# Kernel optimization log

Hardware: AMD Instinct MI355X
Metric: run time of the kernel (lower is better)

## Reference

```python
import jax, jax.numpy as jnp
import numpy as np

WINDOW = 128
LOOK_BACK = 1
LOOK_FWD = 0   # causal=True -> look_forward defaults to 0
DIM = 64       # rotary dim == head dim


def look_around(x, backward=LOOK_BACK, forward=LOOK_FWD, pad_value=-1):
    # x: [b, windows, window, ...]; pad along windows axis, concat along axis 2
    w = x.shape[1]
    pad = [(0, 0), (backward, forward)] + [(0, 0)] * (x.ndim - 2)
    px = jnp.pad(x, pad, constant_values=pad_value)
    return jnp.concatenate([px[:, i:i + w] for i in range(forward + backward + 1)], axis=2)


def rotate_half(x):
    h = (x.shape[-1] + 1) // 2  # ceil split, matches torch .split([ceil, floor])
    x1, x2 = x[..., :h], x[..., h:]
    return jnp.concatenate([-x2, x1], axis=-1)


def setup_inputs() -> dict:
    key = jax.random.key(0)
    kq, kk, kv = jax.random.split(key, 3)
    shape = (4, 16, 4096, 64)
    return {
        "q": jax.random.normal(kq, shape, dtype=jnp.float32),
        "k": jax.random.normal(kk, shape, dtype=jnp.float32),
        "v": jax.random.normal(kv, shape, dtype=jnp.float32),
    }


def reference(q, k, v):
    B, H, T, e = q.shape
    b = B * H
    q, k, v = (t.reshape(b, T, e) for t in (q, k, v))

    # sinusoidal rotary embeddings (start_pos = 0)
    inv_freq = 1.0 / (10000.0 ** (jnp.arange(0, DIM, 2, dtype=jnp.float32) / DIM))
    t_idx = jnp.arange(T, dtype=jnp.float32)
    freqs = jnp.einsum('i,j->ij', t_idx, inv_freq)          # [T, DIM/2]
    emb = jnp.concatenate([freqs, freqs], axis=-1)[:, :DIM][None]  # [1, T, DIM]
    cos, sin = jnp.cos(emb), jnp.sin(emb)
    q = q * cos + rotate_half(q) * sin
    k = k * cos + rotate_half(k) * sin

    # T is a multiple of WINDOW so autopad is a no-op
    w = T // WINDOW
    bq, bk, bv = (t.reshape(b, w, WINDOW, e) for t in (q, k, v))
    bk = look_around(bk)   # [b, w, (LB+LF+1)*WINDOW, e], padded with -1 (masked below)
    bv = look_around(bv)

    b_t = jnp.arange(T).reshape(1, w, WINDOW)
    bq_t = b_t
    bq_k = look_around(b_t)  # [1, w, (LB+LF+1)*WINDOW]

    dots = (jnp.einsum('bwie,bwje->bwij', bq.astype(jnp.float32), bk.astype(jnp.float32))
            * (e ** -0.5)).astype(q.dtype)
    mask_value = -jnp.finfo(dots.dtype).max

    # causal mask (exact_windowsize=False)
    causal_mask = bq_t[:, :, :, None] < bq_k[:, :, None, :]
    dots = jnp.where(causal_mask, mask_value, dots)
    # look-around padding mask
    dots = jnp.where((bq_k == -1)[:, :, None, :], mask_value, dots)

    attn = jax.nn.softmax(dots, axis=-1)
    out = jnp.einsum('bwij,bwje->bwie', attn, bv)
    return out.reshape(B, H, T, e)
```

## Files before the change

### kernel.cpp

```cpp
#include <hip/hip_runtime.h>

#define T_LEN 4096
#define DHEAD 64
#define WINSZ 128
#define KVLEN 256
#define NWIN 32
#define NBH 64
#define FLTMAX 3.402823466e38f

typedef float f32x4 __attribute__((ext_vector_type(4)));
typedef short s16x8 __attribute__((ext_vector_type(8)));
typedef short s16x4 __attribute__((ext_vector_type(4)));

__device__ __forceinline__ unsigned short f2b(float x) {
  unsigned u = __builtin_bit_cast(unsigned, x);
  u += 0x7fffu + ((u >> 16) & 1u);
  return (unsigned short)(u >> 16);
}

__global__ void rope_tab_kernel(float* __restrict__ tab) {
  const int idx = blockIdx.x * 256 + threadIdx.x;
  if (idx >= T_LEN * 32) return;
  const int t = idx >> 5;
  const int i = idx & 31;
  const float freq = powf(10000.0f, -(float)i / 32.0f);
  float s, c;
  sincosf((float)t * freq, &s, &c);
  tab[idx] = c;
  tab[T_LEN * 32 + idx] = s;
}

__global__ __launch_bounds__(512, 4) void lattn_kernel(
    const float* __restrict__ qg, const float* __restrict__ kg,
    const float* __restrict__ vg, const float* __restrict__ tab,
    float* __restrict__ outg) {
  __shared__ __align__(16) unsigned short Kl[KVLEN * DHEAD];
  __shared__ __align__(16) unsigned short Vt[DHEAD * KVLEN];

  const int bid = blockIdx.x;
  const int win = bid & (NWIN - 1);
  const int bh  = bid >> 5;
  const int tid = threadIdx.x;
  const int lane = tid & 63;
  const int wv = tid >> 6;
  const int l15 = lane & 15;
  const int g = lane >> 4;

  const size_t base = (size_t)bh * T_LEN * DHEAD;
  const int q0 = win * WINSZ;
  const int k0 = q0 - WINSZ;
  const bool use_tab = (tab != nullptr);
  const float* ct = tab;
  const float* st = tab + T_LEN * 32;

  {
    const int c = tid & 7;
    const int rr = tid >> 3;
    float fr[4];
    if (!use_tab) {
      #pragma unroll
      for (int j = 0; j < 4; ++j)
        fr[j] = powf(10000.0f, -(float)(4 * c + j) / 32.0f);
    }
    #pragma unroll
    for (int p = 0; p < 4; ++p) {
      const int kr = p * 64 + rr;
      const int kt = k0 + kr;
      float xa[4] = {0.f,0.f,0.f,0.f}, xb[4] = {0.f,0.f,0.f,0.f};
      float cs[4], sn[4];
      #pragma unroll
      for (int j = 0; j < 4; ++j) { cs[j] = 1.f; sn[j] = 0.f; }
      if (kt >= 0) {
        const float* kp = kg + base + (size_t)kt * DHEAD + 4 * c;
        *(float4*)xa = *(const float4*)kp;
        *(float4*)xb = *(const float4*)(kp + 32);
        if (use_tab) {
          *(float4*)cs = *(const float4*)(ct + kt * 32 + 4 * c);
          *(float4*)sn = *(const float4*)(st + kt * 32 + 4 * c);
        } else {
          #pragma unroll
          for (int j = 0; j < 4; ++j) sincosf((float)kt * fr[j], &sn[j], &cs[j]);
        }
      }
      unsigned wlo[2], whi[2];
      #pragma unroll
      for (int h = 0; h < 2; ++h) {
        const int j0 = 2 * h, j1 = 2 * h + 1;
        wlo[h] = (unsigned)f2b(xa[j0]*cs[j0] - xb[j0]*sn[j0]) |
                 ((unsigned)f2b(xa[j1]*cs[j1] - xb[j1]*sn[j1]) << 16);
        whi[h] = (unsigned)f2b(xb[j0]*cs[j0] + xa[j0]*sn[j0]) |
                 ((unsigned)f2b(xb[j1]*cs[j1] + xa[j1]*sn[j1]) << 16);
      }
      const int su = (kr & 7) << 3;
      uint2 a = {wlo[0], wlo[1]}, b = {whi[0], whi[1]};
      *(uint2*)&Kl[kr * 64 + ((4 * c) ^ su)] = a;
      *(uint2*)&Kl[kr * 64 + ((4 * c + 32) ^ su)] = b;
    }
  }

  {
    const int c = tid & 15;
    const int rp = tid >> 4;
    #pragma unroll
    for (int p = 0; p < 4; ++p) {
      const int kr = (p * 32 + rp) * 2;
      const int kt = k0 + kr;
      float va[4] = {0.f,0.f,0.f,0.f}, vb[4] = {0.f,0.f,0.f,0.f};
      if (kt >= 0)
        *(float4*)va = *(const float4*)(vg + base + (size_t)kt * DHEAD + 4 * c);
      if (kt + 1 >= 0)
        *(float4*)vb = *(const float4*)(vg + base + (size_t)(kt + 1) * DHEAD + 4 * c);
      #pragma unroll
      for (int j = 0; j < 4; ++j) {
        const int d = 4 * c + j;
        const unsigned val = (unsigned)f2b(va[j]) | ((unsigned)f2b(vb[j]) << 16);
        *(unsigned*)&Vt[d * 256 + (kr ^ ((d & 7) << 3))] = val;
      }
    }
  }

  s16x8 qa[2];
  {
    const int qrow = q0 + wv * 16 + l15;
    const float* qp = qg + base + (size_t)qrow * DHEAD + 8 * g;
    float xa[8], xb[8], cs[8], sn[8];
    *(float4*)&xa[0] = *(const float4*)qp;
    *(float4*)&xa[4] = *(const float4*)(qp + 4);
    *(float4*)&xb[0] = *(const float4*)(qp + 32);
    *(float4*)&xb[4] = *(const float4*)(qp + 36);
    if (use_tab) {
      const float* cp = ct + qrow * 32 + 8 * g;
      const float* sp = st + qrow * 32 + 8 * g;
      *(float4*)&cs[0] = *(const float4*)cp;
      *(float4*)&cs[4] = *(const float4*)(cp + 4);
      *(float4*)&sn[0] = *(const float4*)sp;
      *(float4*)&sn[4] = *(const float4*)(sp + 4);
    } else {
      #pragma unroll
      for (int j = 0; j < 8; ++j) {
        const float f = powf(10000.0f, -(float)(8 * g + j) / 32.0f);
        sincosf((float)qrow * f, &sn[j], &cs[j]);
      }
    }
    #pragma unroll
    for (int j = 0; j < 8; ++j) {
      qa[0][j] = (short)f2b(xa[j]*cs[j] - xb[j]*sn[j]);
      qa[1][j] = (short)f2b(xb[j]*cs[j] + xa[j]*sn[j]);
    }
  }

  __syncthreads();

  s16x8 pa[8];
  {
    f32x4 acc[16];
    #pragma unroll
    for (int nt = 0; nt < 16; ++nt) acc[nt] = f32x4{0.f, 0.f, 0.f, 0.f};
    #pragma unroll
    for (int nt = 0; nt < 16; ++nt) {
      const int krow = nt * 16 + l15;
      const int su = (krow & 7) << 3;
      const s16x8 k0f = *(const s16x8*)&Kl[krow * 64 + ((8 * g) ^ su)];
      const s16x8 k1f = *(const s16x8*)&Kl[krow * 64 + ((8 * g + 32) ^ su)];
      acc[nt] = __builtin_amdgcn_mfma_f32_16x16x32_bf16(k0f, qa[0], acc[nt], 0, 0, 0);
      acc[nt] = __builtin_amdgcn_mfma_f32_16x16x32_bf16(k1f, qa[1], acc[nt], 0, 0, 0);
    }
    const int qloc = wv * 16 + l15;
    float mx = -FLTMAX;
    #pragma unroll
    for (int nt = 0; nt < 16; ++nt) {
      const bool pad = (win == 0) && (nt < 8);
      #pragma unroll
      for (int r = 0; r < 4; ++r) {
        const int kloc = nt * 16 + 4 * g + r;
        const bool msk = pad || (kloc > WINSZ + qloc);
        const float s = msk ? -FLTMAX : acc[nt][r];
        acc[nt][r] = s;
        mx = fmaxf(mx, s);
      }
    }
    mx = fmaxf(mx, __shfl_xor(mx, 16));
    mx = fmaxf(mx, __shfl_xor(mx, 32));
    float den = 0.f;
    #pragma unroll
    for (int nt = 0; nt < 16; ++nt) {
      #pragma unroll
      for (int r = 0; r < 4; ++r) {
        const float pv = __expf(0.125f * (acc[nt][r] - mx));
        acc[nt][r] = pv;
        den += pv;
      }
    }
    den += __shfl_xor(den, 16);
    den += __shfl_xor(den, 32);
    const float inv = 1.0f / den;
    #pragma unroll
    for (int ks = 0; ks < 8; ++ks) {
      #pragma unroll
      for (int j = 0; j < 4; ++j) {
        pa[ks][j]     = (short)f2b(acc[2 * ks][j] * inv);
        pa[ks][j + 4] = (short)f2b(acc[2 * ks + 1][j] * inv);
      }
    }
  }

  f32x4 oacc[4];
  #pragma unroll
  for (int nt = 0; nt < 4; ++nt) oacc[nt] = f32x4{0.f, 0.f, 0.f, 0.f};

  #pragma unroll
  for (int ks = 0; ks < 8; ++ks) {
    #pragma unroll
    for (int nt = 0; nt < 4; ++nt) {
      const int d = nt * 16 + l15;
      const int su = (d & 7) << 3;
      const int c1 = ks * 32 + 4 * g;
      const s16x4 v0 = *(const s16x4*)&Vt[d * 256 + (c1 ^ su)];
      const s16x4 v1 = *(const s16x4*)&Vt[d * 256 + ((c1 + 16) ^ su)];
      const s16x8 vb = __builtin_shufflevector(v0, v1, 0, 1, 2, 3, 4, 5, 6, 7);
      oacc[nt] = __builtin_amdgcn_mfma_f32_16x16x32_bf16(pa[ks], vb, oacc[nt], 0, 0, 0);
    }
  }

  float* op = outg + base;
  #pragma unroll
  for (int r = 0; r < 4; ++r) {
    const int qrow = q0 + wv * 16 + 4 * g + r;
    #pragma unroll
    for (int nt = 0; nt < 4; ++nt)
      op[(size_t)qrow * DHEAD + nt * 16 + l15] = oacc[nt][r];
  }
}

extern "C" void kernel_launch(void* const* d_in, const int* in_sizes, int n_in,
                              void* d_out, int out_size, void* d_ws, size_t ws_size,
                              hipStream_t stream) {
  (void)in_sizes; (void)n_in; (void)out_size;
  const float* q = (const float*)d_in[0];
  const float* k = (const float*)d_in[1];
  const float* v = (const float*)d_in[2];
  float* out = (float*)d_out;

  float* tab = nullptr;
  const size_t tab_bytes = (size_t)2 * T_LEN * 32 * sizeof(float);
  if (ws_size >= tab_bytes) {
    tab = (float*)d_ws;
    rope_tab_kernel<<<dim3((T_LEN * 32 + 255) / 256), dim3(256), 0, stream>>>(tab);
  }
  lattn_kernel<<<dim3(NBH * NWIN), dim3(512), 0, stream>>>(q, k, v, tab, out);
}
```

Measured before the change: 227.3 us.

## Process four consecutive windows per block, reusing staged K/V halves in a ring

Each block now handles four consecutive windows of one head. It keeps the K/V tiles in two 128-row halves, so only one new half is loaded and converted per window instead of the full 256-row look-around. This removes the duplicate global reads and RoPE/bf16 conversion of the shared previous window. Softmax normalisation is also deferred: the output is scaled at store time instead of scaling the probabilities, the bf16 conversion now uses the library intrinsic, and the V swizzle changed. In exchange the grid has four times fewer blocks, and each window iteration serialises on an extra barrier before reloading.

```diff
diff --git a/kernel.cpp b/kernel.cpp
--- a/kernel.cpp
+++ b/kernel.cpp
@@ -1,11 +1,13 @@
 #include <hip/hip_runtime.h>
+#include <hip/hip_bf16.h>
 
 #define T_LEN 4096
 #define DHEAD 64
 #define WINSZ 128
-#define KVLEN 256
 #define NWIN 32
 #define NBH 64
+#define NWPB 4
+#define NGRP (NWIN / NWPB)
 #define FLTMAX 3.402823466e38f
 
 typedef float f32x4 __attribute__((ext_vector_type(4)));
@@ -13,9 +15,7 @@
 typedef short s16x4 __attribute__((ext_vector_type(4)));
 
 __device__ __forceinline__ unsigned short f2b(float x) {
-  unsigned u = __builtin_bit_cast(unsigned, x);
-  u += 0x7fffu + ((u >> 16) & 1u);
-  return (unsigned short)(u >> 16);
+  return __builtin_bit_cast(unsigned short, __float2bfloat16(x));
 }
 
 __global__ void rope_tab_kernel(float* __restrict__ tab) {
@@ -34,12 +34,12 @@
     const float* __restrict__ qg, const float* __restrict__ kg,
     const float* __restrict__ vg, const float* __restrict__ tab,
     float* __restrict__ outg) {
-  __shared__ __align__(16) unsigned short Kl[KVLEN * DHEAD];
-  __shared__ __align__(16) unsigned short Vt[DHEAD * KVLEN];
+  __shared__ __align__(16) unsigned short Kh[2][WINSZ * DHEAD];
+  __shared__ __align__(16) unsigned short Vh[2][DHEAD * WINSZ];
 
   const int bid = blockIdx.x;
-  const int win = bid & (NWIN - 1);
-  const int bh  = bid >> 5;
+  const int grp = bid & (NGRP - 1);
+  const int bh  = bid >> 3;
   const int tid = threadIdx.x;
   const int lane = tid & 63;
   const int wv = tid >> 6;
@@ -47,188 +47,200 @@
   const int g = lane >> 4;
 
   const size_t base = (size_t)bh * T_LEN * DHEAD;
-  const int q0 = win * WINSZ;
-  const int k0 = q0 - WINSZ;
+  const int win0 = grp * NWPB;
   const bool use_tab = (tab != nullptr);
   const float* ct = tab;
   const float* st = tab + T_LEN * 32;
 
-  {
-    const int c = tid & 7;
-    const int rr = tid >> 3;
-    float fr[4];
-    if (!use_tab) {
-      #pragma unroll
-      for (int j = 0; j < 4; ++j)
-        fr[j] = powf(10000.0f, -(float)(4 * c + j) / 32.0f);
-    }
+  auto stage_half = [&](int hb, int kb) {
+    {
+      const int c = tid & 7;
+      const int rr = tid >> 3;
+      #pragma unroll
+      for (int p = 0; p < 2; ++p) {
+        const int kr = p * 64 + rr;
+        const int kt = kb + kr;
+        float xa[4] = {0.f,0.f,0.f,0.f}, xb[4] = {0.f,0.f,0.f,0.f};
+        float cs[4] = {1.f,1.f,1.f,1.f}, sn[4] = {0.f,0.f,0.f,0.f};
+        if (kt >= 0) {
+          const float* kp = kg + base + (size_t)kt * DHEAD + 4 * c;
+          *(float4*)xa = *(const float4*)kp;
+          *(float4*)xb = *(const float4*)(kp + 32);
+          if (use_tab) {
+            *(float4*)cs = *(const float4*)(ct + kt * 32 + 4 * c);
+            *(float4*)sn = *(const float4*)(st + kt * 32 + 4 * c);
+          } else {
+            #pragma unroll
+            for (int j = 0; j < 4; ++j) {
+              const float f = powf(10000.0f, -(float)(4 * c + j) / 32.0f);
+              sincosf((float)kt * f, &sn[j], &cs[j]);
+            }
+          }
+        }
+        unsigned wlo[2], whi[2];
+        #pragma unroll
+        for (int h = 0; h < 2; ++h) {
+          const int j0 = 2 * h, j1 = 2 * h + 1;
+          wlo[h] = (unsigned)f2b(xa[j0]*cs[j0] - xb[j0]*sn[j0]) |
+                   ((unsigned)f2b(xa[j1]*cs[j1] - xb[j1]*sn[j1]) << 16);
+          whi[h] = (unsigned)f2b(xb[j0]*cs[j0] + xa[j0]*sn[j0]) |
+                   ((unsigned)f2b(xb[j1]*cs[j1] + xa[j1]*sn[j1]) << 16);
+        }
+        const int su = (kr & 7) << 3;
+        *(uint2*)&Kh[hb][kr * 64 + ((4 * c) ^ su)] = uint2{wlo[0], wlo[1]};
+        *(uint2*)&Kh[hb][kr * 64 + ((4 * c + 32) ^ su)] = uint2{whi[0], whi[1]};
+      }
+    }
+    {
+      const int c = tid & 15;
+      const int rp = tid >> 4;
+      #pragma unroll
+      for (int p = 0; p < 2; ++p) {
+        const int kr = (p * 32 + rp) * 2;
+        const int kt = kb + kr;
+        float va[4] = {0.f,0.f,0.f,0.f}, vb[4] = {0.f,0.f,0.f,0.f};
+        if (kt >= 0)
+          *(float4*)va = *(const float4*)(vg + base + (size_t)kt * DHEAD + 4 * c);
+        if (kt + 1 >= 0)
+          *(float4*)vb = *(const float4*)(vg + base + (size_t)(kt + 1) * DHEAD + 4 * c);
+        #pragma unroll
+        for (int j = 0; j < 4; ++j) {
+          const int d = 4 * c + j;
+          const unsigned val = (unsigned)f2b(va[j]) | ((unsigned)f2b(vb[j]) << 16);
+          *(unsigned*)&Vh[hb][d * WINSZ + (kr ^ ((d & 15) << 3))] = val;
+        }
+      }
+    }
+  };
+
+  stage_half(0, win0 * WINSZ - WINSZ);
+  stage_half(1, win0 * WINSZ);
+
+  #pragma unroll 1
+  for (int t = 0; t < NWPB; ++t) {
+    const int win = win0 + t;
+    const int q0 = win * WINSZ;
+    const int pb = t & 1, ob = (t + 1) & 1;
+
+    s16x8 qa0, qa1;
+    {
+      const int qrow = q0 + wv * 16 + l15;
+      const float* qp = qg + base + (size_t)qrow * DHEAD + 8 * g;
+      float xa[8], xb[8], cs[8], sn[8];
+      *(float4*)&xa[0] = *(const float4*)qp;
+      *(float4*)&xa[4] = *(const float4*)(qp + 4);
+      *(float4*)&xb[0] = *(const float4*)(qp + 32);
+      *(float4*)&xb[4] = *(const float4*)(qp + 36);
+      if (use_tab) {
+        const float* cp = ct + qrow * 32 + 8 * g;
+        const float* sp = st + qrow * 32 + 8 * g;
+        *(float4*)&cs[0] = *(const float4*)cp;
+        *(float4*)&cs[4] = *(const float4*)(cp + 4);
+        *(float4*)&sn[0] = *(const float4*)sp;
+        *(float4*)&sn[4] = *(const float4*)(sp + 4);
+      } else {
+        #pragma unroll
+        for (int j = 0; j < 8; ++j) {
+          const float f = powf(10000.0f, -(float)(8 * g + j) / 32.0f);
+          sincosf((float)qrow * f, &sn[j], &cs[j]);
+        }
+      }
+      #pragma unroll
+      for (int j = 0; j < 8; ++j) {
+        qa0[j] = (short)f2b(xa[j]*cs[j] - xb[j]*sn[j]);
+        qa1[j] = (short)f2b(xb[j]*cs[j] + xa[j]*sn[j]);
+      }
+    }
+
+    __syncthreads();
+
+    s16x8 pa[8];
+    float inv;
+    {
+      f32x4 acc[16];
+      #pragma unroll
+      for (int nt = 0; nt < 16; ++nt) acc[nt] = f32x4{0.f, 0.f, 0.f, 0.f};
+      #pragma unroll
+      for (int nt = 0; nt < 16; ++nt) {
+        const int hb = (nt < 8) ? pb : ob;
+        const int krh = (nt & 7) * 16 + l15;
+        const int su = (krh & 7) << 3;
+        const s16x8 k0f = *(const s16x8*)&Kh[hb][krh * 64 + ((8 * g) ^ su)];
+        const s16x8 k1f = *(const s16x8*)&Kh[hb][krh * 64 + ((8 * g + 32) ^ su)];
+        acc[nt] = __builtin_amdgcn_mfma_f32_16x16x32_bf16(k0f, qa0, acc[nt], 0, 0, 0);
+        acc[nt] = __builtin_amdgcn_mfma_f32_16x16x32_bf16(k1f, qa1, acc[nt], 0, 0, 0);
+      }
+      const int qloc = wv * 16 + l15;
+      float mx = -FLTMAX;
+      #pragma unroll
+      for (int nt = 0; nt < 16; ++nt) {
+        const bool pad = (win == 0) && (nt < 8);
+        #pragma unroll
+        for (int r = 0; r < 4; ++r) {
+          const int kloc = nt * 16 + 4 * g + r;
+          const bool msk = pad || (kloc > WINSZ + qloc);
+          const float s = msk ? -FLTMAX : acc[nt][r];
+          acc[nt][r] = s;
+          mx = fmaxf(mx, s);
+        }
+      }
+      mx = fmaxf(mx, __shfl_xor(mx, 16));
+      mx = fmaxf(mx, __shfl_xor(mx, 32));
+      float den = 0.f;
+      #pragma unroll
+      for (int nt = 0; nt < 16; ++nt) {
+        #pragma unroll
+        for (int r = 0; r < 4; ++r) {
+          const float pv = __expf(0.125f * (acc[nt][r] - mx));
+          acc[nt][r] = pv;
+          den += pv;
+        }
+      }
+      den += __shfl_xor(den, 16);
+      den += __shfl_xor(den, 32);
+      inv = 1.0f / den;
+      #pragma unroll
+      for (int ks = 0; ks < 8; ++ks) {
+        #pragma unroll
+        for (int j = 0; j < 4; ++j) {
+          pa[ks][j]     = (short)f2b(acc[2 * ks][j]);
+          pa[ks][j + 4] = (short)f2b(acc[2 * ks + 1][j]);
+        }
+      }
+    }
+
+    f32x4 oacc[4];
     #pragma unroll
-    for (int p = 0; p < 4; ++p) {
-      const int kr = p * 64 + rr;
-      const int kt = k0 + kr;
-      float xa[4] = {0.f,0.f,0.f,0.f}, xb[4] = {0.f,0.f,0.f,0.f};
-      float cs[4], sn[4];
-      #pragma unroll
-      for (int j = 0; j < 4; ++j) { cs[j] = 1.f; sn[j] = 0.f; }
-      if (kt >= 0) {
-        const float* kp = kg + base + (size_t)kt * DHEAD + 4 * c;
-        *(float4*)xa = *(const float4*)kp;
-        *(float4*)xb = *(const float4*)(kp + 32);
-        if (use_tab) {
-          *(float4*)cs = *(const float4*)(ct + kt * 32 + 4 * c);
-          *(float4*)sn = *(const float4*)(st + kt * 32 + 4 * c);
-        } else {
-          #pragma unroll
-          for (int j = 0; j < 4; ++j) sincosf((float)kt * fr[j], &sn[j], &cs[j]);
-        }
-      }
-      unsigned wlo[2], whi[2];
-      #pragma unroll
-      for (int h = 0; h < 2; ++h) {
-        const int j0 = 2 * h, j1 = 2 * h + 1;
-        wlo[h] = (unsigned)f2b(xa[j0]*cs[j0] - xb[j0]*sn[j0]) |
-                 ((unsigned)f2b(xa[j1]*cs[j1] - xb[j1]*sn[j1]) << 16);
-        whi[h] = (unsigned)f2b(xb[j0]*cs[j0] + xa[j0]*sn[j0]) |
-                 ((unsigned)f2b(xb[j1]*cs[j1] + xa[j1]*sn[j1]) << 16);
-      }
-      const int su = (kr & 7) << 3;
-      uint2 a = {wlo[0], wlo[1]}, b = {whi[0], whi[1]};
-      *(uint2*)&Kl[kr * 64 + ((4 * c) ^ su)] = a;
-      *(uint2*)&Kl[kr * 64 + ((4 * c + 32) ^ su)] = b;
-    }
-  }
-
-  {
-    const int c = tid & 15;
-    const int rp = tid >> 4;
-    #pragma unroll
-    for (int p = 0; p < 4; ++p) {
-      const int kr = (p * 32 + rp) * 2;
-      const int kt = k0 + kr;
-      float va[4] = {0.f,0.f,0.f,0.f}, vb[4] = {0.f,0.f,0.f,0.f};
-      if (kt >= 0)
-        *(float4*)va = *(const float4*)(vg + base + (size_t)kt * DHEAD + 4 * c);
-      if (kt + 1 >= 0)
-        *(float4*)vb = *(const float4*)(vg + base + (size_t)(kt + 1) * DHEAD + 4 * c);
-      #pragma unroll
-      for (int j = 0; j < 4; ++j) {
-        const int d = 4 * c + j;
-        const unsigned val = (unsigned)f2b(va[j]) | ((unsigned)f2b(vb[j]) << 16);
-        *(unsigned*)&Vt[d * 256 + (kr ^ ((d & 7) << 3))] = val;
-      }
-    }
-  }
-
-  s16x8 qa[2];
-  {
-    const int qrow = q0 + wv * 16 + l15;
-    const float* qp = qg + base + (size_t)qrow * DHEAD + 8 * g;
-    float xa[8], xb[8], cs[8], sn[8];
-    *(float4*)&xa[0] = *(const float4*)qp;
-    *(float4*)&xa[4] = *(const float4*)(qp + 4);
-    *(float4*)&xb[0] = *(const float4*)(qp + 32);
-    *(float4*)&xb[4] = *(const float4*)(qp + 36);
-    if (use_tab) {
-      const float* cp = ct + qrow * 32 + 8 * g;
-      const float* sp = st + qrow * 32 + 8 * g;
-      *(float4*)&cs[0] = *(const float4*)cp;
-      *(float4*)&cs[4] = *(const float4*)(cp + 4);
-      *(float4*)&sn[0] = *(const float4*)sp;
-      *(float4*)&sn[4] = *(const float4*)(sp + 4);
-    } else {
-      #pragma unroll
-      for (int j = 0; j < 8; ++j) {
-        const float f = powf(10000.0f, -(float)(8 * g + j) / 32.0f);
-        sincosf((float)qrow * f, &sn[j], &cs[j]);
-      }
-    }
-    #pragma unroll
-    for (int j = 0; j < 8; ++j) {
-      qa[0][j] = (short)f2b(xa[j]*cs[j] - xb[j]*sn[j]);
-      qa[1][j] = (short)f2b(xb[j]*cs[j] + xa[j]*sn[j]);
-    }
-  }
-
-  __syncthreads();
-
-  s16x8 pa[8];
-  {
-    f32x4 acc[16];
-    #pragma unroll
-    for (int nt = 0; nt < 16; ++nt) acc[nt] = f32x4{0.f, 0.f, 0.f, 0.f};
-    #pragma unroll
-    for (int nt = 0; nt < 16; ++nt) {
-      const int krow = nt * 16 + l15;
-      const int su = (krow & 7) << 3;
-      const s16x8 k0f = *(const s16x8*)&Kl[krow * 64 + ((8 * g) ^ su)];
-      const s16x8 k1f = *(const s16x8*)&Kl[krow * 64 + ((8 * g + 32) ^ su)];
-      acc[nt] = __builtin_amdgcn_mfma_f32_16x16x32_bf16(k0f, qa[0], acc[nt], 0, 0, 0);
-      acc[nt] = __builtin_amdgcn_mfma_f32_16x16x32_bf16(k1f, qa[1], acc[nt], 0, 0, 0);
-    }
-    const int qloc = wv * 16 + l15;
-    float mx = -FLTMAX;
-    #pragma unroll
-    for (int nt = 0; nt < 16; ++nt) {
-      const bool pad = (win == 0) && (nt < 8);
-      #pragma unroll
-      for (int r = 0; r < 4; ++r) {
-        const int kloc = nt * 16 + 4 * g + r;
-        const bool msk = pad || (kloc > WINSZ + qloc);
-        const float s = msk ? -FLTMAX : acc[nt][r];
-        acc[nt][r] = s;
-        mx = fmaxf(mx, s);
-      }
-    }
-    mx = fmaxf(mx, __shfl_xor(mx, 16));
-    mx = fmaxf(mx, __shfl_xor(mx, 32));
-    float den = 0.f;
-    #pragma unroll
-    for (int nt = 0; nt < 16; ++nt) {
-      #pragma unroll
-      for (int r = 0; r < 4; ++r) {
-        const float pv = __expf(0.125f * (acc[nt][r] - mx));
-        acc[nt][r] = pv;
-        den += pv;
-      }
-    }
-    den += __shfl_xor(den, 16);
-    den += __shfl_xor(den, 32);
-    const float inv = 1.0f / den;
+    for (int nt = 0; nt < 4; ++nt) oacc[nt] = f32x4{0.f, 0.f, 0.f, 0.f};
     #pragma unroll
     for (int ks = 0; ks < 8; ++ks) {
-      #pragma unroll
-      for (int j = 0; j < 4; ++j) {
-        pa[ks][j]     = (short)f2b(acc[2 * ks][j] * inv);
-        pa[ks][j + 4] = (short)f2b(acc[2 * ks + 1][j] * inv);
-      }
-    }
-  }
-
-  f32x4 oacc[4];
-  #pragma unroll
-  for (int nt = 0; nt < 4; ++nt) oacc[nt] = f32x4{0.f, 0.f, 0.f, 0.f};
-
-  #pragma unroll
-  for (int ks = 0; ks < 8; ++ks) {
+      const int hb = (ks < 4) ? pb : ob;
+      const int c1 = (ks & 3) * 32 + 4 * g;
+      #pragma unroll
+      for (int nt = 0; nt < 4; ++nt) {
+        const int d = nt * 16 + l15;
+        const int su = (d & 15) << 3;
+        const s16x4 v0 = *(const s16x4*)&Vh[hb][d * WINSZ + (c1 ^ su)];
+        const s16x4 v1 = *(const s16x4*)&Vh[hb][d * WINSZ + ((c1 + 16) ^ su)];
+        const s16x8 vb = __builtin_shufflevector(v0, v1, 0, 1, 2, 3, 4, 5, 6, 7);
+        oacc[nt] = __builtin_amdgcn_mfma_f32_16x16x32_bf16(pa[ks], vb, oacc[nt], 0, 0, 0);
+      }
+    }
+
+    float* op = outg + base;
     #pragma unroll
-    for (int nt = 0; nt < 4; ++nt) {
-      const int d = nt * 16 + l15;
-      const int su = (d & 7) << 3;
-      const int c1 = ks * 32 + 4 * g;
-      const s16x4 v0 = *(const s16x4*)&Vt[d * 256 + (c1 ^ su)];
-      const s16x4 v1 = *(const s16x4*)&Vt[d * 256 + ((c1 + 16) ^ su)];
-      const s16x8 vb = __builtin_shufflevector(v0, v1, 0, 1, 2, 3, 4, 5, 6, 7);
-      oacc[nt] = __builtin_amdgcn_mfma_f32_16x16x32_bf16(pa[ks], vb, oacc[nt], 0, 0, 0);
-    }
-  }
-
-  float* op = outg + base;
-  #pragma unroll
-  for (int r = 0; r < 4; ++r) {
-    const int qrow = q0 + wv * 16 + 4 * g + r;
-    #pragma unroll
-    for (int nt = 0; nt < 4; ++nt)
-      op[(size_t)qrow * DHEAD + nt * 16 + l15] = oacc[nt][r];
+    for (int r = 0; r < 4; ++r) {
+      const float ir = __shfl(inv, 4 * g + r, 64);
+      const int qrow = q0 + wv * 16 + 4 * g + r;
+      #pragma unroll
+      for (int nt = 0; nt < 4; ++nt)
+        op[(size_t)qrow * DHEAD + nt * 16 + l15] = oacc[nt][r] * ir;
+    }
+
+    if (t + 1 < NWPB) {
+      __syncthreads();
+      stage_half(t & 1, (win + 1) * WINSZ);
+    }
   }
 }
 
@@ -247,5 +259,5 @@
     tab = (float*)d_ws;
     rope_tab_kernel<<<dim3((T_LEN * 32 + 255) / 256), dim3(256), 0, stream>>>(tab);
   }
-  lattn_kernel<<<dim3(NBH * NWIN), dim3(512), 0, stream>>>(q, k, v, tab, out);
-}
+  lattn_kernel<<<dim3(NBH * NGRP), dim3(512), 0, stream>>>(q, k, v, tab, out);
+}
```

Result: slower. 253.7 us (+11.6%).
